# Optimization experiments

Hardware: AMD Instinct MI355X
Metric: run time of the kernel (lower is better)

Reference implementation:

```python
import jax, jax.numpy as jnp
import numpy as np

B, V, C, T = 8, 2048, 32, 32


def setup_inputs() -> dict:
    key = jax.random.key(0)
    ks = jax.random.split(key, 26)
    f32 = jnp.float32

    def w(k, shape, fan_in):
        # torch-style U(-1/sqrt(fan), 1/sqrt(fan)) init, kept small to avoid gate saturation
        s = 1.0 / np.sqrt(fan_in)
        return jax.random.uniform(k, shape, f32, -s, s)

    inp = {
        "Mvv": (jax.random.uniform(ks[0], (B, V, V)) < 0.01).astype(f32),
        "n_colors": jax.random.randint(ks[1], (B,), 1, C + 1, jnp.int32),
        "vh0": jax.random.normal(ks[2], (2, B, V), f32),   # Normal(0,1) per stacked vertex cell
        "ch0": jax.random.uniform(ks[3], (B, C), f32),      # Uniform(0,1)
        # vertex LSTM cell 0: input 2V, hidden V
        "v0_wih": w(ks[4], (4 * V, 2 * V), V), "v0_whh": w(ks[5], (4 * V, V), V),
        "v0_bih": w(ks[6], (4 * V,), V), "v0_bhh": w(ks[7], (4 * V,), V),
        # vertex LSTM cell 1: input V, hidden V
        "v1_wih": w(ks[8], (4 * V, V), V), "v1_whh": w(ks[9], (4 * V, V), V),
        "v1_bih": w(ks[10], (4 * V,), V), "v1_bhh": w(ks[11], (4 * V,), V),
        # color LSTM cell: input C, hidden C
        "c_wih": w(ks[12], (4 * C, C), C), "c_whh": w(ks[13], (4 * C, C), C),
        "c_bih": w(ks[14], (4 * C,), C), "c_bhh": w(ks[15], (4 * C,), C),
        # message / vote MLPs
        "cmsg_w": w(ks[16], (C, C), C), "cmsg_b": w(ks[17], (C,), C),
        "vmsg_w": w(ks[18], (V, V), V), "vmsg_b": w(ks[19], (V,), V),
        "vote_w": w(ks[20], (V, V), V), "vote_b": w(ks[21], (V,), V),
    }
    return inp


def _lstm_cell(x, h, c, wih, whh, bih, bhh):
    # PyTorch LSTMCell: gates in i, f, g, o order
    gates = x @ wih.T + h @ whh.T + bih + bhh
    i, f, g, o = jnp.split(gates, 4, axis=-1)
    c_new = jax.nn.sigmoid(f) * c + jax.nn.sigmoid(i) * jnp.tanh(g)
    h_new = jax.nn.sigmoid(o) * jnp.tanh(c_new)
    return h_new, c_new


def reference(Mvv, n_colors, vh0, ch0,
              v0_wih, v0_whh, v0_bih, v0_bhh,
              v1_wih, v1_whh, v1_bih, v1_bhh,
              c_wih, c_whh, c_bih, c_bhh,
              cmsg_w, cmsg_b, vmsg_w, vmsg_b, vote_w, vote_b):
    # Mvc[b, v, j] = 1 if j < n_colors[b] -> rows identical across v; represent as mask [B, C]
    mask = (jnp.arange(C)[None, :] < n_colors[:, None]).astype(Mvv.dtype)

    def step(carry, _):
        h0, m0, h1, m1, ch, cm = carry
        color_msg = jax.nn.relu(ch @ cmsg_w.T + cmsg_b)           # [B, C]
        vertex_msg = jax.nn.relu(h1 @ vmsg_w.T + vmsg_b)          # [B, V]
        # Mvc @ color_msg: every vertex row of Mvc equals mask[b] -> scalar per batch, broadcast over V
        s_c = jnp.sum(mask * color_msg, axis=-1, keepdims=True)   # [B, 1]
        muled_c_msg = jnp.broadcast_to(s_c, (B, V))               # [B, V]
        muled_v = jnp.einsum('buv,bv->bu', Mvv, h1)               # adjacency message passing
        x0 = jnp.concatenate([muled_c_msg, muled_v], axis=1)      # [B, 2V]
        # Mvc^T @ vertex_msg: sum over vertices, masked over colors
        rnn_color_in = mask * jnp.sum(vertex_msg, axis=-1, keepdims=True)  # [B, C]
        # dropout (p=0.3) is identity in eval mode
        h0, m0 = _lstm_cell(x0, h0, m0, v0_wih, v0_whh, v0_bih, v0_bhh)
        h1, m1 = _lstm_cell(h0, h1, m1, v1_wih, v1_whh, v1_bih, v1_bhh)
        ch, cm = _lstm_cell(rnn_color_in, ch, cm, c_wih, c_whh, c_bih, c_bhh)
        return (h0, m0, h1, m1, ch, cm), None

    zV = jnp.zeros((B, V), Mvv.dtype)
    zC = jnp.zeros((B, C), Mvv.dtype)
    carry0 = (vh0[0], zV, vh0[1], zV, ch0, zC)
    carry, _ = jax.lax.scan(step, carry0, None, length=T)
    h1 = carry[2]
    vote = jax.nn.sigmoid(h1 @ vote_w.T + vote_b)                 # [B, V]
    pred = jax.nn.sigmoid(jnp.mean(vote, axis=1))                 # [B]
    return pred
```

## Files before the change

### kernel.cpp

```cpp
#include <hip/hip_runtime.h>
#include <math.h>

#define BB 8
#define VV 2048
#define CC 32
#define TT 32
#define JJ 8192

typedef unsigned short u16;
typedef unsigned int u32;
typedef short short8 __attribute__((ext_vector_type(8)));
typedef float f32x4 __attribute__((ext_vector_type(4)));

struct P {
  const float* Mvv; const int* ncol; const float* vh0; const float* ch0;
  const float* v0_wih; const float* v0_whh; const float* v0_bih; const float* v0_bhh;
  const float* v1_wih; const float* v1_whh; const float* v1_bih; const float* v1_bhh;
  const float* c_wih; const float* c_whh; const float* c_bih; const float* c_bhh;
  const float* cmsg_w; const float* cmsg_b; const float* vmsg_w; const float* vmsg_b;
  const float* vote_w; const float* vote_b;
  u16* w0xP; u16* w0hP; u16* w1xP; u16* w1hP; u16* wvP;
  u16* h0A; u16* h1A; u16* mvA;
  float* rs0; int* adj_cnt; int* adj_cols;
  float* m0; float* h1; float* m1; float* chb; float* cm;
  float* g0p; float* g1p; float* p1p; float* vmp; float* pacc;
  float* out;
};

__device__ __forceinline__ u16 f2bf(float f) {
  u32 x = __float_as_uint(f);
  u32 r = (x + 0x7fffu + ((x >> 16) & 1u)) >> 16;
  return (u16)r;
}

__device__ __forceinline__ float sigm(float x) { return 1.f / (1.f + expf(-x)); }


__global__ __launch_bounds__(256) void kPack(const float* __restrict__ src, int stride, int colOff,
                                             u16* __restrict__ dst) {
  int tile = blockIdx.x * 4 + (threadIdx.x >> 6);
  int lane = threadIdx.x & 63;
  int jt = tile >> 6, kt = tile & 63;
  int j = jt * 16 + (lane & 15);
  int k = colOff + kt * 32 + ((lane >> 4) << 3);
  const float* sp = src + (size_t)j * stride + k;
  float4 a = *(const float4*)sp;
  float4 b = *(const float4*)(sp + 4);
  uint4 pk;
  pk.x = (u32)f2bf(a.x) | ((u32)f2bf(a.y) << 16);
  pk.y = (u32)f2bf(a.z) | ((u32)f2bf(a.w) << 16);
  pk.z = (u32)f2bf(b.x) | ((u32)f2bf(b.y) << 16);
  pk.w = (u32)f2bf(b.z) | ((u32)f2bf(b.w) << 16);
  *(uint4*)(dst + (size_t)tile * 512 + lane * 8) = pk;
}

__global__ __launch_bounds__(256) void kRs0(P p) {
  int wid = threadIdx.x >> 6, lane = threadIdx.x & 63;
  int row = blockIdx.x * 4 + wid;
  const float* sp = p.v0_wih + (size_t)row * (2 * VV);
  float s = 0.f;
  for (int i = lane; i < VV; i += 64) s += sp[i];
#pragma unroll
  for (int d = 32; d > 0; d >>= 1) s += __shfl_down(s, d, 64);
  if (lane == 0) p.rs0[row] = s;
}

__global__ __launch_bounds__(256) void kAdj(P p) {
  int wid = threadIdx.x >> 6, lane = threadIdx.x & 63;
  int row = blockIdx.x * 4 + wid;
  const float* mp = p.Mvv + (size_t)row * VV;
  int* cols = p.adj_cols + (size_t)row * 64;
  int cnt = 0;
  for (int it = 0; it < 32; ++it) {
    float v = mp[it * 64 + lane];
    bool nz = v > 0.5f;
    unsigned long long mk = __ballot(nz);
    if (nz) {
      int pos = cnt + (int)__popcll(mk & ((1ull << lane) - 1ull));
      if (pos < 64) cols[pos] = it * 64 + lane;
    }
    cnt += (int)__popcll(mk);
  }
  if (lane == 0) p.adj_cnt[row] = cnt > 64 ? 64 : cnt;
}

__device__ __forceinline__ u32 apack_slot(const float* __restrict__ X, int slot) {
  int kt = slot >> 8;
  int r = slot & 255;
  int lane = r >> 2, w = r & 3;
  int b = lane & 15;
  if (b >= 8) return 0u;
  int k = kt * 32 + ((lane >> 4) << 3) + w * 2;
  return (u32)f2bf(X[b * VV + k]) | ((u32)f2bf(X[b * VV + k + 1]) << 16);
}

__global__ __launch_bounds__(256) void kInit(P p) {
  int i = blockIdx.x * 256 + threadIdx.x;
  p.m0[i] = 0.f; p.m1[i] = 0.f;
  p.h1[i] = p.vh0[BB * VV + i];
  ((u32*)p.h0A)[i] = apack_slot(p.vh0, i);
  ((u32*)p.h1A)[i] = apack_slot(p.vh0 + BB * VV, i);
  ((u32*)p.mvA)[i] = 0u;
  if (i < BB * CC) { p.chb[i] = p.ch0[i]; p.cm[i] = 0.f; }
  if (i < 8) p.pacc[i] = 0.f;
}

__device__ __forceinline__ void apack_write(u16* __restrict__ A, int b, int u, float v) {
  int kt = u >> 5, sub = (u >> 3) & 3, i = u & 7;
  A[((size_t)(kt * 64 + sub * 16 + b)) * 8 + i] = f2bf(v);
}


__global__ __launch_bounds__(256) void kG(P p) {
  int flat = blockIdx.x * 256 + threadIdx.x;
  int b = flat >> 11, u = flat & 2047;
  int cnt = p.adj_cnt[flat];
  const int* cp = p.adj_cols + (size_t)flat * 64;
  const float* hb = p.h1 + b * VV;
  float s = 0.f;
  for (int q = 0; q < cnt; ++q) s += hb[cp[q]];
  apack_write(p.mvA, b, u, s);
}

__device__ __forceinline__ void mma_chunk(const short8* __restrict__ ap,
                                          const short8* __restrict__ bp,
                                          f32x4& acc) {
#pragma unroll 4
  for (int kt = 0; kt < 16; ++kt) {
    short8 a = ap[(size_t)kt * 64];
    short8 b = bp[(size_t)kt * 64];
    acc = __builtin_amdgcn_mfma_f32_16x16x32_bf16(a, b, acc, 0, 0, 0);
  }
}

__device__ __forceinline__ void store_part(float* __restrict__ out, int OJ,
                                           int jt, int lane, f32x4 acc) {
  int n = lane & 15, rq = lane >> 4;
  if (rq < 2) {
    float* op = out + (size_t)(rq * 4) * OJ + jt * 16 + n;
#pragma unroll
    for (int r = 0; r < 4; ++r) op[(size_t)r * OJ] = acc[r];
  }
}

__global__ __launch_bounds__(256) void kA(P p) {
  int bx = blockIdx.x, tid = threadIdx.x;
  int wv_ = tid >> 6, lane = tid & 63;
  f32x4 acc = {0.f, 0.f, 0.f, 0.f};
  if (bx < 512) {
    int s = bx & 3, jb = bx >> 2;
    int jt = jb * 4 + wv_;
    int ktb = s * 16;
    mma_chunk((const short8*)p.mvA + (size_t)ktb * 64 + lane,
              (const short8*)p.w0xP + ((size_t)jt * 64 + ktb) * 64 + lane, acc);
    mma_chunk((const short8*)p.h0A + (size_t)ktb * 64 + lane,
              (const short8*)p.w0hP + ((size_t)jt * 64 + ktb) * 64 + lane, acc);
    store_part(p.g0p + (size_t)s * BB * JJ, JJ, jt, lane, acc);
  } else if (bx < 1024) {
    int i = bx - 512; int s = i & 3, jb = i >> 2;
    int jt = jb * 4 + wv_;
    int ktb = s * 16;
    mma_chunk((const short8*)p.h1A + (size_t)ktb * 64 + lane,
              (const short8*)p.w1hP + ((size_t)jt * 64 + ktb) * 64 + lane, acc);
    store_part(p.p1p + (size_t)s * BB * JJ, JJ, jt, lane, acc);
  } else {
    int i = bx - 1024; int s = i & 3, jb = i >> 2;
    int jt = jb * 4 + wv_;
    int ktb = s * 16;
    mma_chunk((const short8*)p.h1A + (size_t)ktb * 64 + lane,
              (const short8*)p.wvP + ((size_t)jt * 64 + ktb) * 64 + lane, acc);
    store_part(p.vmp + (size_t)s * BB * VV, VV, jt, lane, acc);
  }
}

__global__ __launch_bounds__(256) void kB(P p, int t) {
  int bx = blockIdx.x, tid = threadIdx.x;
  const float* chp = p.chb + (t & 1) * BB * CC;
  float* chq = p.chb + ((t + 1) & 1) * BB * CC;
  if (bx < 64) {
    __shared__ float scv[BB];
    __shared__ float scs[BB * CC];
    {
      int b = tid >> 5, jc = tid & 31;
      float a = p.cmsg_b[jc];
#pragma unroll
      for (int k = 0; k < 32; ++k) a += chp[b * CC + k] * p.cmsg_w[jc * CC + k];
      a = fmaxf(a, 0.f);
      scs[tid] = (jc < p.ncol[b]) ? a : 0.f;
    }
    __syncthreads();
    if (tid < 8) {
      float s = 0.f;
      for (int jc = 0; jc < 32; ++jc) s += scs[tid * 32 + jc];
      scv[tid] = s;
    }
    __syncthreads();
    int flat = bx * 256 + tid;
    int b = flat >> 11, u = flat & 2047;
    float g4[4];
#pragma unroll
    for (int g = 0; g < 4; ++g) {
      int jj = g * 2048 + u;
      float s = p.v0_bih[jj] + p.v0_bhh[jj] + scv[b] * p.rs0[jj];
      const float* gp = p.g0p + (size_t)b * JJ + jj;
#pragma unroll
      for (int sl = 0; sl < 4; ++sl) s += gp[(size_t)sl * BB * JJ];
      g4[g] = s;
    }
    float ig = sigm(g4[0]), fg = sigm(g4[1]), gg = tanhf(g4[2]), og = sigm(g4[3]);
    float mn = fg * p.m0[flat] + ig * gg;
    float hn = og * tanhf(mn);
    p.m0[flat] = mn;
    apack_write(p.h0A, b, u, hn);
  } else {
    __shared__ float red[256];
    __shared__ float vs[BB];
    for (int b = 0; b < 8; ++b) {
      float ps = 0.f;
      for (int uu = tid; uu < VV; uu += 256) {
        float s = p.vmsg_b[uu];
        const float* vp = p.vmp + (size_t)b * VV + uu;
#pragma unroll
        for (int sl = 0; sl < 4; ++sl) s += vp[(size_t)sl * BB * VV];
        ps += fmaxf(s, 0.f);
      }
      red[tid] = ps;
      __syncthreads();
      for (int d = 128; d > 0; d >>= 1) {
        if (tid < d) red[tid] += red[tid + d];
        __syncthreads();
      }
      if (tid == 0) vs[b] = red[0];
      __syncthreads();
    }
    int b = tid >> 5, tc = tid & 31;
    int nc = p.ncol[b];
    float g4[4];
#pragma unroll
    for (int g = 0; g < 4; ++g) {
      int jc = g * 32 + tc;
      float s = p.c_bih[jc] + p.c_bhh[jc];
      float wsum = 0.f;
      for (int k = 0; k < nc; ++k) wsum += p.c_wih[jc * CC + k];
      s += vs[b] * wsum;
#pragma unroll
      for (int k = 0; k < 32; ++k) s += chp[b * CC + k] * p.c_whh[jc * CC + k];
      g4[g] = s;
    }
    float ig = sigm(g4[0]), fg = sigm(g4[1]), gg = tanhf(g4[2]), og = sigm(g4[3]);
    float mn = fg * p.cm[tid] + ig * gg;
    float hn = og * tanhf(mn);
    p.cm[tid] = mn; chq[tid] = hn;
  }
}

__global__ __launch_bounds__(256) void kC(P p) {
  int bx = blockIdx.x, tid = threadIdx.x;
  int wv_ = tid >> 6, lane = tid & 63;
  int s = bx & 3, jb = bx >> 2;
  int jt = jb * 4 + wv_;
  int ktb = s * 16;
  f32x4 acc = {0.f, 0.f, 0.f, 0.f};
  mma_chunk((const short8*)p.h0A + (size_t)ktb * 64 + lane,
            (const short8*)p.w1xP + ((size_t)jt * 64 + ktb) * 64 + lane, acc);
  store_part(p.g1p + (size_t)s * BB * JJ, JJ, jt, lane, acc);
}

__global__ __launch_bounds__(256) void kD(P p) {
  int bx = blockIdx.x, tid = threadIdx.x;
  int flat = bx * 256 + tid;
  int b = flat >> 11, u = flat & 2047;
  float g4[4];
#pragma unroll
  for (int g = 0; g < 4; ++g) {
    int jj = g * 2048 + u;
    float s = p.v1_bih[jj] + p.v1_bhh[jj];
    const float* gp = p.g1p + (size_t)b * JJ + jj;
    const float* pp = p.p1p + (size_t)b * JJ + jj;
#pragma unroll
    for (int sl = 0; sl < 4; ++sl) s += gp[(size_t)sl * BB * JJ] + pp[(size_t)sl * BB * JJ];
    g4[g] = s;
  }
  float ig = sigm(g4[0]), fg = sigm(g4[1]), gg = tanhf(g4[2]), og = sigm(g4[3]);
  float mn = fg * p.m1[flat] + ig * gg;
  float hn = og * tanhf(mn);
  p.m1[flat] = mn; p.h1[flat] = hn;
  apack_write(p.h1A, b, u, hn);
}

__global__ __launch_bounds__(256) void kV1(P p) {
  int bx = blockIdx.x, tid = threadIdx.x;
  int b = bx >> 3, ut = bx & 7;
  int u = ut * 256 + tid;
  __shared__ float hs[VV];
  for (int i = tid; i < VV; i += 256) hs[i] = p.h1[b * VV + i];
  __syncthreads();
  const float* wr = p.vote_w + (size_t)u * VV;
  float s = p.vote_b[u];
  for (int k = 0; k < VV; k += 4) {
    float4 w = *(const float4*)(wr + k);
    s += w.x * hs[k] + w.y * hs[k + 1] + w.z * hs[k + 2] + w.w * hs[k + 3];
  }
  atomicAdd(&p.pacc[b], sigm(s));
}

__global__ __launch_bounds__(64) void kV2(P p) {
  int tid = threadIdx.x;
  if (tid < 8) p.out[tid] = sigm(p.pacc[tid] * (1.f / (float)VV));
}

extern "C" void kernel_launch(void* const* d_in, const int* in_sizes, int n_in,
                              void* d_out, int out_size, void* d_ws, size_t ws_size,
                              hipStream_t stream) {
  P p;
  p.Mvv    = (const float*)d_in[0];
  p.ncol   = (const int*)d_in[1];
  p.vh0    = (const float*)d_in[2];
  p.ch0    = (const float*)d_in[3];
  p.v0_wih = (const float*)d_in[4];
  p.v0_whh = (const float*)d_in[5];
  p.v0_bih = (const float*)d_in[6];
  p.v0_bhh = (const float*)d_in[7];
  p.v1_wih = (const float*)d_in[8];
  p.v1_whh = (const float*)d_in[9];
  p.v1_bih = (const float*)d_in[10];
  p.v1_bhh = (const float*)d_in[11];
  p.c_wih  = (const float*)d_in[12];
  p.c_whh  = (const float*)d_in[13];
  p.c_bih  = (const float*)d_in[14];
  p.c_bhh  = (const float*)d_in[15];
  p.cmsg_w = (const float*)d_in[16];
  p.cmsg_b = (const float*)d_in[17];
  p.vmsg_w = (const float*)d_in[18];
  p.vmsg_b = (const float*)d_in[19];
  p.vote_w = (const float*)d_in[20];
  p.vote_b = (const float*)d_in[21];

  char* w = (char*)d_ws;
  size_t o = 0;
  auto alloc = [&](size_t bytes) -> void* {
    void* r = w + o;
    o = (o + bytes + 255) & ~(size_t)255;
    return r;
  };
  p.w0xP = (u16*)alloc((size_t)512 * 64 * 1024);
  p.w0hP = (u16*)alloc((size_t)512 * 64 * 1024);
  p.w1xP = (u16*)alloc((size_t)512 * 64 * 1024);
  p.w1hP = (u16*)alloc((size_t)512 * 64 * 1024);
  p.wvP  = (u16*)alloc((size_t)128 * 64 * 1024);
  p.h0A  = (u16*)alloc(64 * 1024);
  p.h1A  = (u16*)alloc(64 * 1024);
  p.mvA  = (u16*)alloc(64 * 1024);
  p.rs0 = (float*)alloc(JJ * 4);
  p.adj_cnt  = (int*)alloc((size_t)BB * VV * 4);
  p.adj_cols = (int*)alloc((size_t)BB * VV * 64 * 4);
  p.m0 = (float*)alloc((size_t)BB * VV * 4);
  p.h1 = (float*)alloc((size_t)BB * VV * 4);
  p.m1 = (float*)alloc((size_t)BB * VV * 4);
  p.chb = (float*)alloc(2 * BB * CC * 4);
  p.cm  = (float*)alloc(BB * CC * 4);
  p.g0p = (float*)alloc((size_t)4 * BB * JJ * 4);
  p.g1p = (float*)alloc((size_t)4 * BB * JJ * 4);
  p.p1p = (float*)alloc((size_t)4 * BB * JJ * 4);
  p.vmp = (float*)alloc((size_t)4 * BB * VV * 4);
  p.pacc = (float*)alloc(256);
  p.out = (float*)d_out;

  kPack<<<8192, 256, 0, stream>>>(p.v0_wih, 2 * VV, VV, p.w0xP);
  kPack<<<8192, 256, 0, stream>>>(p.v0_whh, VV, 0, p.w0hP);
  kPack<<<8192, 256, 0, stream>>>(p.v1_wih, VV, 0, p.w1xP);
  kPack<<<8192, 256, 0, stream>>>(p.v1_whh, VV, 0, p.w1hP);
  kPack<<<2048, 256, 0, stream>>>(p.vmsg_w, VV, 0, p.wvP);
  kRs0<<<2048, 256, 0, stream>>>(p);
  kAdj<<<4096, 256, 0, stream>>>(p);
  kInit<<<64, 256, 0, stream>>>(p);

  for (int t = 0; t < TT; ++t) {
    kG<<<64, 256, 0, stream>>>(p);
    kA<<<1152, 256, 0, stream>>>(p);
    kB<<<65, 256, 0, stream>>>(p, t);
    kC<<<512, 256, 0, stream>>>(p);
    kD<<<64, 256, 0, stream>>>(p);
  }
  kV1<<<64, 256, 0, stream>>>(p);
  kV2<<<1, 64, 0, stream>>>(p);
}
```

Before: 3.040 ms.

## Fuse recurrent loop into one persistent kernel with software grid barriers

Replaces the per-timestep launches (five kernels times 32 steps plus the vote kernels) with one persistent kernel of 256 blocks that synchronises through an atomic grid barrier. Each block now covers the full K range of its matmul tile, so the split-K partial buffers go away and the LSTM gate math is fused right after the MFMA through shared memory. The vote projection is also moved to bf16 MFMA and the biases are pre-summed. The risk is that correctness depends on all 256 blocks being co-resident, and each block now does a longer serial K loop, which lowers parallelism.

Measured after the change: 4.980 ms. +63.8%, slower.

```diff
diff --git a/kernel.cpp b/kernel.cpp
--- a/kernel.cpp
+++ b/kernel.cpp
@@ -6,6 +6,7 @@
 #define CC 32
 #define TT 32
 #define JJ 8192
+#define NBLK 256
 
 typedef unsigned short u16;
 typedef unsigned int u32;
@@ -19,11 +20,12 @@
   const float* c_wih; const float* c_whh; const float* c_bih; const float* c_bhh;
   const float* cmsg_w; const float* cmsg_b; const float* vmsg_w; const float* vmsg_b;
   const float* vote_w; const float* vote_b;
-  u16* w0xP; u16* w0hP; u16* w1xP; u16* w1hP; u16* wvP;
-  u16* h0A; u16* h1A; u16* mvA;
-  float* rs0; int* adj_cnt; int* adj_cols;
-  float* m0; float* h1; float* m1; float* chb; float* cm;
-  float* g0p; float* g1p; float* p1p; float* vmp; float* pacc;
+  u16 *w0xP, *w0hP, *w1xP, *w1hP, *wvP, *wvoteP;
+  u16 *h0A, *h1A, *mvA;
+  float *rs0, *bias0, *bias1;
+  int *adj_cnt, *adj_cols;
+  float *m0, *h1, *m1, *ch, *cm, *p1p, *scv, *vsum, *pacc;
+  int* bar;
   float* out;
 };
 
@@ -32,7 +34,6 @@
   u32 r = (x + 0x7fffu + ((x >> 16) & 1u)) >> 16;
   return (u16)r;
 }
-
 __device__ __forceinline__ float sigm(float x) { return 1.f / (1.f + expf(-x)); }
 
 
@@ -94,6 +95,11 @@
   return (u32)f2bf(X[b * VV + k]) | ((u32)f2bf(X[b * VV + k + 1]) << 16);
 }
 
+__device__ __forceinline__ void apack_write(u16* __restrict__ A, int b, int u, float v) {
+  int kt = u >> 5, sub = (u >> 3) & 3, i = u & 7;
+  A[((size_t)(kt * 64 + sub * 16 + b)) * 8 + i] = f2bf(v);
+}
+
 __global__ __launch_bounds__(256) void kInit(P p) {
   int i = blockIdx.x * 256 + threadIdx.x;
   p.m0[i] = 0.f; p.m1[i] = 0.f;
@@ -101,212 +107,203 @@
   ((u32*)p.h0A)[i] = apack_slot(p.vh0, i);
   ((u32*)p.h1A)[i] = apack_slot(p.vh0 + BB * VV, i);
   ((u32*)p.mvA)[i] = 0u;
-  if (i < BB * CC) { p.chb[i] = p.ch0[i]; p.cm[i] = 0.f; }
-  if (i < 8) p.pacc[i] = 0.f;
-}
-
-__device__ __forceinline__ void apack_write(u16* __restrict__ A, int b, int u, float v) {
-  int kt = u >> 5, sub = (u >> 3) & 3, i = u & 7;
-  A[((size_t)(kt * 64 + sub * 16 + b)) * 8 + i] = f2bf(v);
-}
-
-
-__global__ __launch_bounds__(256) void kG(P p) {
-  int flat = blockIdx.x * 256 + threadIdx.x;
-  int b = flat >> 11, u = flat & 2047;
-  int cnt = p.adj_cnt[flat];
-  const int* cp = p.adj_cols + (size_t)flat * 64;
-  const float* hb = p.h1 + b * VV;
-  float s = 0.f;
-  for (int q = 0; q < cnt; ++q) s += hb[cp[q]];
-  apack_write(p.mvA, b, u, s);
-}
-
-__device__ __forceinline__ void mma_chunk(const short8* __restrict__ ap,
-                                          const short8* __restrict__ bp,
-                                          f32x4& acc) {
+  if (i < JJ) { p.bias0[i] = p.v0_bih[i] + p.v0_bhh[i]; p.bias1[i] = p.v1_bih[i] + p.v1_bhh[i]; }
+  if (i < BB * CC) { p.ch[i] = p.ch0[i]; p.cm[i] = 0.f; }
+  if (i < 8) { p.pacc[i] = 0.f; p.vsum[i] = 0.f; p.scv[i] = 0.f; }
+  if (i < 2) p.bar[i] = 0;
+}
+
+
+__device__ __forceinline__ void gridbar(int* bar) {
+  __syncthreads();
+  if (threadIdx.x == 0) {
+    __threadfence();
+    int g = __hip_atomic_load(&bar[1], __ATOMIC_RELAXED, __HIP_MEMORY_SCOPE_AGENT);
+    int old = __hip_atomic_fetch_add(&bar[0], 1, __ATOMIC_ACQ_REL, __HIP_MEMORY_SCOPE_AGENT);
+    if (old == NBLK - 1) {
+      __hip_atomic_store(&bar[0], 0, __ATOMIC_RELAXED, __HIP_MEMORY_SCOPE_AGENT);
+      __hip_atomic_fetch_add(&bar[1], 1, __ATOMIC_RELEASE, __HIP_MEMORY_SCOPE_AGENT);
+    } else {
+      while (__hip_atomic_load(&bar[1], __ATOMIC_RELAXED, __HIP_MEMORY_SCOPE_AGENT) == g)
+        __builtin_amdgcn_s_sleep(2);
+    }
+    __threadfence();
+  }
+  __syncthreads();
+}
+
+__device__ __forceinline__ f32x4 mma_dual(const short8* __restrict__ a0, const short8* __restrict__ b0,
+                                          const short8* __restrict__ a1, const short8* __restrict__ b1) {
+  f32x4 c0 = {0.f, 0.f, 0.f, 0.f}, c1 = c0, c2 = c0, c3 = c0;
 #pragma unroll 4
-  for (int kt = 0; kt < 16; ++kt) {
-    short8 a = ap[(size_t)kt * 64];
-    short8 b = bp[(size_t)kt * 64];
-    acc = __builtin_amdgcn_mfma_f32_16x16x32_bf16(a, b, acc, 0, 0, 0);
-  }
-}
-
-__device__ __forceinline__ void store_part(float* __restrict__ out, int OJ,
-                                           int jt, int lane, f32x4 acc) {
-  int n = lane & 15, rq = lane >> 4;
-  if (rq < 2) {
-    float* op = out + (size_t)(rq * 4) * OJ + jt * 16 + n;
-#pragma unroll
-    for (int r = 0; r < 4; ++r) op[(size_t)r * OJ] = acc[r];
-  }
-}
-
-__global__ __launch_bounds__(256) void kA(P p) {
-  int bx = blockIdx.x, tid = threadIdx.x;
-  int wv_ = tid >> 6, lane = tid & 63;
-  f32x4 acc = {0.f, 0.f, 0.f, 0.f};
-  if (bx < 512) {
-    int s = bx & 3, jb = bx >> 2;
-    int jt = jb * 4 + wv_;
-    int ktb = s * 16;
-    mma_chunk((const short8*)p.mvA + (size_t)ktb * 64 + lane,
-              (const short8*)p.w0xP + ((size_t)jt * 64 + ktb) * 64 + lane, acc);
-    mma_chunk((const short8*)p.h0A + (size_t)ktb * 64 + lane,
-              (const short8*)p.w0hP + ((size_t)jt * 64 + ktb) * 64 + lane, acc);
-    store_part(p.g0p + (size_t)s * BB * JJ, JJ, jt, lane, acc);
-  } else if (bx < 1024) {
-    int i = bx - 512; int s = i & 3, jb = i >> 2;
-    int jt = jb * 4 + wv_;
-    int ktb = s * 16;
-    mma_chunk((const short8*)p.h1A + (size_t)ktb * 64 + lane,
-              (const short8*)p.w1hP + ((size_t)jt * 64 + ktb) * 64 + lane, acc);
-    store_part(p.p1p + (size_t)s * BB * JJ, JJ, jt, lane, acc);
-  } else {
-    int i = bx - 1024; int s = i & 3, jb = i >> 2;
-    int jt = jb * 4 + wv_;
-    int ktb = s * 16;
-    mma_chunk((const short8*)p.h1A + (size_t)ktb * 64 + lane,
-              (const short8*)p.wvP + ((size_t)jt * 64 + ktb) * 64 + lane, acc);
-    store_part(p.vmp + (size_t)s * BB * VV, VV, jt, lane, acc);
-  }
-}
-
-__global__ __launch_bounds__(256) void kB(P p, int t) {
-  int bx = blockIdx.x, tid = threadIdx.x;
-  const float* chp = p.chb + (t & 1) * BB * CC;
-  float* chq = p.chb + ((t + 1) & 1) * BB * CC;
-  if (bx < 64) {
-    __shared__ float scv[BB];
-    __shared__ float scs[BB * CC];
-    {
+  for (int kt = 0; kt < 32; ++kt) {
+    c0 = __builtin_amdgcn_mfma_f32_16x16x32_bf16(a0[kt * 64], b0[kt * 64], c0, 0, 0, 0);
+    c1 = __builtin_amdgcn_mfma_f32_16x16x32_bf16(a0[(kt + 32) * 64], b0[(kt + 32) * 64], c1, 0, 0, 0);
+    c2 = __builtin_amdgcn_mfma_f32_16x16x32_bf16(a1[kt * 64], b1[kt * 64], c2, 0, 0, 0);
+    c3 = __builtin_amdgcn_mfma_f32_16x16x32_bf16(a1[(kt + 32) * 64], b1[(kt + 32) * 64], c3, 0, 0, 0);
+  }
+  return (c0 + c1) + (c2 + c3);
+}
+
+__device__ __forceinline__ f32x4 mma_one(const short8* __restrict__ a, const short8* __restrict__ b) {
+  f32x4 c0 = {0.f, 0.f, 0.f, 0.f}, c1 = c0;
+#pragma unroll 8
+  for (int kt = 0; kt < 32; ++kt) {
+    c0 = __builtin_amdgcn_mfma_f32_16x16x32_bf16(a[kt * 64], b[kt * 64], c0, 0, 0, 0);
+    c1 = __builtin_amdgcn_mfma_f32_16x16x32_bf16(a[(kt + 32) * 64], b[(kt + 32) * 64], c1, 0, 0, 0);
+  }
+  return c0 + c1;
+}
+
+__global__ __launch_bounds__(256, 2) void kMain(P p) {
+  const int bx = blockIdx.x, tid = threadIdx.x;
+  const int wvid = tid >> 6, lane = tid & 63;
+  const int n = lane & 15, rq = lane >> 4;
+  __shared__ float smem[512];
+
+  for (int t = 0; t < TT; ++t) {
+    if (bx < 64) {
+      int flat = (bx << 8) + tid, b = flat >> 11;
+      int cnt = p.adj_cnt[flat];
+      const int* cp = p.adj_cols + (size_t)flat * 64;
+      const float* hb = p.h1 + (b << 11);
+      float s = 0.f;
+      for (int q = 0; q < cnt; ++q) s += hb[cp[q]];
+      apack_write(p.mvA, b, flat & 2047, s);
+    } else if (bx == NBLK - 1) {
       int b = tid >> 5, jc = tid & 31;
       float a = p.cmsg_b[jc];
-#pragma unroll
-      for (int k = 0; k < 32; ++k) a += chp[b * CC + k] * p.cmsg_w[jc * CC + k];
+      const float* chb = p.ch + b * CC;
+#pragma unroll
+      for (int k = 0; k < CC; ++k) a += chb[k] * p.cmsg_w[jc * CC + k];
       a = fmaxf(a, 0.f);
-      scs[tid] = (jc < p.ncol[b]) ? a : 0.f;
-    }
-    __syncthreads();
-    if (tid < 8) {
-      float s = 0.f;
-      for (int jc = 0; jc < 32; ++jc) s += scs[tid * 32 + jc];
-      scv[tid] = s;
-    }
-    __syncthreads();
-    int flat = bx * 256 + tid;
-    int b = flat >> 11, u = flat & 2047;
-    float g4[4];
-#pragma unroll
-    for (int g = 0; g < 4; ++g) {
-      int jj = g * 2048 + u;
-      float s = p.v0_bih[jj] + p.v0_bhh[jj] + scv[b] * p.rs0[jj];
-      const float* gp = p.g0p + (size_t)b * JJ + jj;
-#pragma unroll
-      for (int sl = 0; sl < 4; ++sl) s += gp[(size_t)sl * BB * JJ];
-      g4[g] = s;
-    }
-    float ig = sigm(g4[0]), fg = sigm(g4[1]), gg = tanhf(g4[2]), og = sigm(g4[3]);
-    float mn = fg * p.m0[flat] + ig * gg;
-    float hn = og * tanhf(mn);
-    p.m0[flat] = mn;
-    apack_write(p.h0A, b, u, hn);
-  } else {
-    __shared__ float red[256];
-    __shared__ float vs[BB];
-    for (int b = 0; b < 8; ++b) {
-      float ps = 0.f;
-      for (int uu = tid; uu < VV; uu += 256) {
-        float s = p.vmsg_b[uu];
-        const float* vp = p.vmp + (size_t)b * VV + uu;
-#pragma unroll
-        for (int sl = 0; sl < 4; ++sl) s += vp[(size_t)sl * BB * VV];
-        ps += fmaxf(s, 0.f);
-      }
-      red[tid] = ps;
+      smem[tid] = (jc < p.ncol[b]) ? a : 0.f;
       __syncthreads();
-      for (int d = 128; d > 0; d >>= 1) {
-        if (tid < d) red[tid] += red[tid + d];
-        __syncthreads();
-      }
-      if (tid == 0) vs[b] = red[0];
+      if (tid < 8) {
+        float s = 0.f;
+        for (int j2 = 0; j2 < 32; ++j2) s += smem[tid * 32 + j2];
+        p.scv[tid] = s; p.vsum[tid] = 0.f;
+      }
+    }
+    gridbar(p.bar);
+    if (bx < 128) {
+      int jt = wvid * 128 + bx;
+      f32x4 acc = mma_dual((const short8*)p.mvA + lane,
+                           (const short8*)p.w0xP + (size_t)jt * 4096 + lane,
+                           (const short8*)p.h0A + lane,
+                           (const short8*)p.w0hP + (size_t)jt * 4096 + lane);
+      if (rq < 2) {
+#pragma unroll
+        for (int r = 0; r < 4; ++r) smem[(wvid * 8 + rq * 4 + r) * 16 + n] = acc[r];
+      }
       __syncthreads();
-    }
-    int b = tid >> 5, tc = tid & 31;
-    int nc = p.ncol[b];
-    float g4[4];
-#pragma unroll
-    for (int g = 0; g < 4; ++g) {
-      int jc = g * 32 + tc;
-      float s = p.c_bih[jc] + p.c_bhh[jc];
-      float wsum = 0.f;
-      for (int k = 0; k < nc; ++k) wsum += p.c_wih[jc * CC + k];
-      s += vs[b] * wsum;
-#pragma unroll
-      for (int k = 0; k < 32; ++k) s += chp[b * CC + k] * p.c_whh[jc * CC + k];
-      g4[g] = s;
-    }
-    float ig = sigm(g4[0]), fg = sigm(g4[1]), gg = tanhf(g4[2]), og = sigm(g4[3]);
-    float mn = fg * p.cm[tid] + ig * gg;
-    float hn = og * tanhf(mn);
-    p.cm[tid] = mn; chq[tid] = hn;
-  }
-}
-
-__global__ __launch_bounds__(256) void kC(P p) {
-  int bx = blockIdx.x, tid = threadIdx.x;
-  int wv_ = tid >> 6, lane = tid & 63;
-  int s = bx & 3, jb = bx >> 2;
-  int jt = jb * 4 + wv_;
-  int ktb = s * 16;
-  f32x4 acc = {0.f, 0.f, 0.f, 0.f};
-  mma_chunk((const short8*)p.h0A + (size_t)ktb * 64 + lane,
-            (const short8*)p.w1xP + ((size_t)jt * 64 + ktb) * 64 + lane, acc);
-  store_part(p.g1p + (size_t)s * BB * JJ, JJ, jt, lane, acc);
-}
-
-__global__ __launch_bounds__(256) void kD(P p) {
-  int bx = blockIdx.x, tid = threadIdx.x;
-  int flat = bx * 256 + tid;
-  int b = flat >> 11, u = flat & 2047;
-  float g4[4];
-#pragma unroll
-  for (int g = 0; g < 4; ++g) {
-    int jj = g * 2048 + u;
-    float s = p.v1_bih[jj] + p.v1_bhh[jj];
-    const float* gp = p.g1p + (size_t)b * JJ + jj;
-    const float* pp = p.p1p + (size_t)b * JJ + jj;
-#pragma unroll
-    for (int sl = 0; sl < 4; ++sl) s += gp[(size_t)sl * BB * JJ] + pp[(size_t)sl * BB * JJ];
-    g4[g] = s;
-  }
-  float ig = sigm(g4[0]), fg = sigm(g4[1]), gg = tanhf(g4[2]), og = sigm(g4[3]);
-  float mn = fg * p.m1[flat] + ig * gg;
-  float hn = og * tanhf(mn);
-  p.m1[flat] = mn; p.h1[flat] = hn;
-  apack_write(p.h1A, b, u, hn);
-}
-
-__global__ __launch_bounds__(256) void kV1(P p) {
-  int bx = blockIdx.x, tid = threadIdx.x;
-  int b = bx >> 3, ut = bx & 7;
-  int u = ut * 256 + tid;
-  __shared__ float hs[VV];
-  for (int i = tid; i < VV; i += 256) hs[i] = p.h1[b * VV + i];
-  __syncthreads();
-  const float* wr = p.vote_w + (size_t)u * VV;
-  float s = p.vote_b[u];
-  for (int k = 0; k < VV; k += 4) {
-    float4 w = *(const float4*)(wr + k);
-    s += w.x * hs[k] + w.y * hs[k + 1] + w.z * hs[k + 2] + w.w * hs[k + 3];
-  }
-  atomicAdd(&p.pacc[b], sigm(s));
-}
-
-__global__ __launch_bounds__(64) void kV2(P p) {
-  int tid = threadIdx.x;
-  if (tid < 8) p.out[tid] = sigm(p.pacc[tid] * (1.f / (float)VV));
+      if (tid < 128) {
+        int b = tid >> 4, u16i = tid & 15, u = bx * 16 + u16i, flat = (b << 11) + u;
+        float sv = p.scv[b];
+        float g0 = smem[(0 * 8 + b) * 16 + u16i] + p.bias0[u]        + sv * p.rs0[u];
+        float g1 = smem[(1 * 8 + b) * 16 + u16i] + p.bias0[2048 + u] + sv * p.rs0[2048 + u];
+        float g2 = smem[(2 * 8 + b) * 16 + u16i] + p.bias0[4096 + u] + sv * p.rs0[4096 + u];
+        float g3 = smem[(3 * 8 + b) * 16 + u16i] + p.bias0[6144 + u] + sv * p.rs0[6144 + u];
+        float mn = sigm(g1) * p.m0[flat] + sigm(g0) * tanhf(g2);
+        float hn = sigm(g3) * tanhf(mn);
+        p.m0[flat] = mn;
+        apack_write(p.h0A, b, u, hn);
+      }
+    } else {
+      int jt = ((bx - 128) << 2) + wvid;
+      f32x4 acc = mma_one((const short8*)p.h1A + lane,
+                          (const short8*)p.w1hP + (size_t)jt * 4096 + lane);
+      if (rq < 2) {
+        float* op = p.p1p + (size_t)(rq * 4) * JJ + jt * 16 + n;
+#pragma unroll
+        for (int r = 0; r < 4; ++r) op[(size_t)r * JJ] = acc[r];
+      }
+      if (bx < 160) {
+        int jv = ((bx - 128) << 2) + wvid;
+        f32x4 av = mma_one((const short8*)p.h1A + lane,
+                           (const short8*)p.wvP + (size_t)jv * 4096 + lane);
+        float vals[4];
+#pragma unroll
+        for (int r = 0; r < 4; ++r)
+          vals[r] = (rq < 2) ? fmaxf(av[r] + p.vmsg_b[jv * 16 + n], 0.f) : 0.f;
+#pragma unroll
+        for (int m = 1; m < 16; m <<= 1) {
+#pragma unroll
+          for (int r = 0; r < 4; ++r) vals[r] += __shfl_xor(vals[r], m, 64);
+        }
+        if (n == 0 && rq < 2) {
+#pragma unroll
+          for (int r = 0; r < 4; ++r) atomicAdd(&p.vsum[rq * 4 + r], vals[r]);
+        }
+      }
+    }
+    gridbar(p.bar);
+    if (bx < 128) {
+      int jt = wvid * 128 + bx;
+      f32x4 acc = mma_one((const short8*)p.h0A + lane,
+                          (const short8*)p.w1xP + (size_t)jt * 4096 + lane);
+      if (rq < 2) {
+#pragma unroll
+        for (int r = 0; r < 4; ++r) acc[r] += p.p1p[(size_t)(rq * 4 + r) * JJ + jt * 16 + n];
+#pragma unroll
+        for (int r = 0; r < 4; ++r) smem[(wvid * 8 + rq * 4 + r) * 16 + n] = acc[r];
+      }
+      __syncthreads();
+      if (tid < 128) {
+        int b = tid >> 4, u16i = tid & 15, u = bx * 16 + u16i, flat = (b << 11) + u;
+        float g0 = smem[(0 * 8 + b) * 16 + u16i] + p.bias1[u];
+        float g1 = smem[(1 * 8 + b) * 16 + u16i] + p.bias1[2048 + u];
+        float g2 = smem[(2 * 8 + b) * 16 + u16i] + p.bias1[4096 + u];
+        float g3 = smem[(3 * 8 + b) * 16 + u16i] + p.bias1[6144 + u];
+        float mn = sigm(g1) * p.m1[flat] + sigm(g0) * tanhf(g2);
+        float hn = sigm(g3) * tanhf(mn);
+        p.m1[flat] = mn; p.h1[flat] = hn;
+        apack_write(p.h1A, b, u, hn);
+      }
+    } else if (bx == 128) {
+      int b = tid >> 5, jc = tid & 31;
+      int nc = p.ncol[b];
+      float vb = p.vsum[b];
+      const float* chb = p.ch + b * CC;
+      float g4[4];
+#pragma unroll
+      for (int g = 0; g < 4; ++g) {
+        int j = g * CC + jc;
+        float s = p.c_bih[j] + p.c_bhh[j];
+        float ws = 0.f;
+        for (int k = 0; k < nc; ++k) ws += p.c_wih[j * CC + k];
+        s += vb * ws;
+#pragma unroll
+        for (int k = 0; k < CC; ++k) s += chb[k] * p.c_whh[j * CC + k];
+        g4[g] = s;
+      }
+      __syncthreads();
+      float mn = sigm(g4[1]) * p.cm[tid] + sigm(g4[0]) * tanhf(g4[2]);
+      float hn = sigm(g4[3]) * tanhf(mn);
+      p.cm[tid] = mn; p.ch[tid] = hn;
+    }
+    gridbar(p.bar);
+  }
+  if (bx < 32) {
+    int jv = (bx << 2) + wvid;
+    f32x4 av = mma_one((const short8*)p.h1A + lane,
+                       (const short8*)p.wvoteP + (size_t)jv * 4096 + lane);
+    float vals[4];
+#pragma unroll
+    for (int r = 0; r < 4; ++r)
+      vals[r] = (rq < 2) ? sigm(av[r] + p.vote_b[jv * 16 + n]) : 0.f;
+#pragma unroll
+    for (int m = 1; m < 16; m <<= 1) {
+#pragma unroll
+      for (int r = 0; r < 4; ++r) vals[r] += __shfl_xor(vals[r], m, 64);
+    }
+    if (n == 0 && rq < 2) {
+#pragma unroll
+      for (int r = 0; r < 4; ++r) atomicAdd(&p.pacc[rq * 4 + r], vals[r]);
+    }
+  }
+  gridbar(p.bar);
+  if (bx == 0 && tid < 8) p.out[tid] = sigm(p.pacc[tid] * (1.f / (float)VV));
 }
 
 extern "C" void kernel_launch(void* const* d_in, const int* in_sizes, int n_in,
@@ -347,23 +344,26 @@
   p.w0hP = (u16*)alloc((size_t)512 * 64 * 1024);
   p.w1xP = (u16*)alloc((size_t)512 * 64 * 1024);
   p.w1hP = (u16*)alloc((size_t)512 * 64 * 1024);
-  p.wvP  = (u16*)alloc((size_t)128 * 64 * 1024);
+  p.wvP    = (u16*)alloc((size_t)128 * 64 * 1024);
+  p.wvoteP = (u16*)alloc((size_t)128 * 64 * 1024);
   p.h0A  = (u16*)alloc(64 * 1024);
   p.h1A  = (u16*)alloc(64 * 1024);
   p.mvA  = (u16*)alloc(64 * 1024);
-  p.rs0 = (float*)alloc(JJ * 4);
+  p.rs0   = (float*)alloc(JJ * 4);
+  p.bias0 = (float*)alloc(JJ * 4);
+  p.bias1 = (float*)alloc(JJ * 4);
   p.adj_cnt  = (int*)alloc((size_t)BB * VV * 4);
   p.adj_cols = (int*)alloc((size_t)BB * VV * 64 * 4);
   p.m0 = (float*)alloc((size_t)BB * VV * 4);
   p.h1 = (float*)alloc((size_t)BB * VV * 4);
   p.m1 = (float*)alloc((size_t)BB * VV * 4);
-  p.chb = (float*)alloc(2 * BB * CC * 4);
-  p.cm  = (float*)alloc(BB * CC * 4);
-  p.g0p = (float*)alloc((size_t)4 * BB * JJ * 4);
-  p.g1p = (float*)alloc((size_t)4 * BB * JJ * 4);
-  p.p1p = (float*)alloc((size_t)4 * BB * JJ * 4);
-  p.vmp = (float*)alloc((size_t)4 * BB * VV * 4);
+  p.ch = (float*)alloc(BB * CC * 4);
+  p.cm = (float*)alloc(BB * CC * 4);
+  p.p1p = (float*)alloc((size_t)BB * JJ * 4);
+  p.scv  = (float*)alloc(256);
+  p.vsum = (float*)alloc(256);
   p.pacc = (float*)alloc(256);
+  p.bar  = (int*)alloc(256);
   p.out = (float*)d_out;
 
   kPack<<<8192, 256, 0, stream>>>(p.v0_wih, 2 * VV, VV, p.w0xP);
@@ -371,17 +371,10 @@
   kPack<<<8192, 256, 0, stream>>>(p.v1_wih, VV, 0, p.w1xP);
   kPack<<<8192, 256, 0, stream>>>(p.v1_whh, VV, 0, p.w1hP);
   kPack<<<2048, 256, 0, stream>>>(p.vmsg_w, VV, 0, p.wvP);
+  kPack<<<2048, 256, 0, stream>>>(p.vote_w, VV, 0, p.wvoteP);
   kRs0<<<2048, 256, 0, stream>>>(p);
   kAdj<<<4096, 256, 0, stream>>>(p);
   kInit<<<64, 256, 0, stream>>>(p);
 
-  for (int t = 0; t < TT; ++t) {
-    kG<<<64, 256, 0, stream>>>(p);
-    kA<<<1152, 256, 0, stream>>>(p);
-    kB<<<65, 256, 0, stream>>>(p, t);
-    kC<<<512, 256, 0, stream>>>(p);
-    kD<<<64, 256, 0, stream>>>(p);
-  }
-  kV1<<<64, 256, 0, stream>>>(p);
-  kV2<<<1, 64, 0, stream>>>(p);
-}
+  kMain<<<NBLK, 256, 0, stream>>>(p);
+}
```
